# Kernel optimization log

Hardware: AMD Instinct MI355X
Metric: run time of the kernel (lower is better)

Reference implementation:

```python
import jax, jax.numpy as jnp
import numpy as np
import math

B, L, D, H, DFF = 2, 2048, 1024, 16, 4096

def _mha(xq, xkv, Wq, bq, Wk, bk, Wv, bv, Wo, bo, mask, h):
    # xq: [B,Lq,D], xkv: [B,Lk,D], mask: [B,1,Lq,Lk] bool
    b, lq, d = xq.shape
    dk = d // h
    q = (xq @ Wq + bq).reshape(b, lq, h, dk).transpose(0, 2, 1, 3)        # [B,h,Lq,dk]
    k = (xkv @ Wk + bk).reshape(b, -1, h, dk).transpose(0, 2, 1, 3)       # [B,h,Lk,dk]
    v = (xkv @ Wv + bv).reshape(b, -1, h, dk).transpose(0, 2, 1, 3)       # [B,h,Lk,dk]
    scores = jnp.einsum('bhqd,bhkd->bhqk', q, k) / jnp.sqrt(jnp.float32(dk))
    scores = jnp.where(mask, scores, jnp.float32(-1e9))                   # masked_fill(mask==0, -1e9)
    prob = jax.nn.softmax(scores, axis=-1)
    out = jnp.einsum('bhqk,bhkd->bhqd', prob, v)
    out = out.transpose(0, 2, 1, 3).reshape(b, lq, d)
    return out @ Wo + bo

def setup_inputs() -> dict:
    key = jax.random.key(0)
    ks = jax.random.split(key, 16)
    s = 0.02
    inp = {
        'tgt': jax.random.normal(ks[0], (B, L, D), jnp.float32),
        'encoder_out': jax.random.normal(ks[1], (B, L, D), jnp.float32),
        'tgt_mask': jnp.broadcast_to(jnp.tril(jnp.ones((L, L), bool)), (B, 1, L, L)),
        'src_tgt_mask': jnp.ones((B, 1, L, L), bool),
    }
    names = ['sWq','sWk','sWv','sWo','cWq','cWk','cWv','cWo']
    for i, n in enumerate(names):
        inp[n] = s * jax.random.normal(ks[2 + i], (D, D), jnp.float32)
        inp['sb' + n[2] if n[0] == 's' else 'cb' + n[2]] = jnp.zeros((D,), jnp.float32)
    inp['W1'] = s * jax.random.normal(ks[10], (D, DFF), jnp.float32)
    inp['b1'] = jnp.zeros((DFF,), jnp.float32)
    inp['W2'] = s * jax.random.normal(ks[11], (DFF, D), jnp.float32)
    inp['b2'] = jnp.zeros((D,), jnp.float32)
    return inp

def reference(tgt, encoder_out, tgt_mask, src_tgt_mask,
              sWq, sbq, sWk, sbk, sWv, sbv, sWo, sbo,
              cWq, cbq, cWk, cbk, cWv, cbv, cWo, cbo,
              W1, b1, W2, b2):
    # residual 1: masked self-attention (no norm)
    x = tgt + _mha(tgt, tgt, sWq, sbq, sWk, sbk, sWv, sbv, sWo, sbo, tgt_mask, H)
    # residual 2: cross-attention over encoder_out
    x = x + _mha(x, encoder_out, cWq, cbq, cWk, cbk, cWv, cbv, cWo, cbo, src_tgt_mask, H)
    # residual 3: position-wise FFN with ReLU
    x = x + (jax.nn.relu(x @ W1 + b1) @ W2 + b2)
    return x
```

## Files before the change

### kernel.cpp

```cpp
#include <hip/hip_runtime.h>

typedef unsigned short u16;
typedef unsigned int u32;
typedef __attribute__((ext_vector_type(8))) short short8;
typedef __attribute__((ext_vector_type(8))) __bf16 bf16x8;
typedef __attribute__((ext_vector_type(4))) float f32x4;
typedef __attribute__((ext_vector_type(4))) u16 u16x4;
typedef __attribute__((ext_vector_type(2))) u32 u32x2;

#define GLD16(gp, lp) __builtin_amdgcn_global_load_lds( \
    (const __attribute__((address_space(1))) unsigned int*)(gp), \
    (__attribute__((address_space(3))) unsigned int*)(lp), 16, 0, 0)

#if defined(__has_builtin) && __has_builtin(__builtin_amdgcn_exp2f)
#define EXP2(x) __builtin_amdgcn_exp2f(x)
#else
static __device__ __forceinline__ float exp2_asm(float x){
  float r; asm("v_exp_f32 %0, %1" : "=v"(r) : "v"(x)); return r;
}
#define EXP2(x) exp2_asm(x)
#endif

__device__ __forceinline__ float bf2f(u16 u){
  unsigned x = ((unsigned)u) << 16; float f; __builtin_memcpy(&f, &x, 4); return f;
}
__device__ __forceinline__ u16 f2bf(float f){
  unsigned x; __builtin_memcpy(&x, &f, 4);
  x += 0x7fffu + ((x >> 16) & 1u);
  return (u16)(x >> 16);
}
__device__ __forceinline__ u32 pkhi(float lo, float hi){
  u32 a, b; __builtin_memcpy(&a, &lo, 4); __builtin_memcpy(&b, &hi, 4);
  return __builtin_amdgcn_perm(b, a, 0x07060302u);
}
__device__ __forceinline__ f32x4 mfma_bf16(short8 a, short8 b, f32x4 c){
  return __builtin_amdgcn_mfma_f32_16x16x32_bf16(
      __builtin_bit_cast(bf16x8, a), __builtin_bit_cast(bf16x8, b), c, 0, 0, 0);
}

__global__ __launch_bounds__(256) void k_conv(const float* __restrict__ s, u16* __restrict__ d, int n){
  int i4 = (blockIdx.x * 256 + threadIdx.x) * 4;
  if (i4 < n){
    float4 v = *(const float4*)(s + i4);
    u16x4 o; o.x = f2bf(v.x); o.y = f2bf(v.y); o.z = f2bf(v.z); o.w = f2bf(v.w);
    *(u16x4*)(d + i4) = o;
  }
}

__global__ __launch_bounds__(256) void k_transpose(const float* __restrict__ s, u16* __restrict__ d, int K, int N){
  __shared__ float t[32][33];
  int bx = blockIdx.x * 32, by = blockIdx.y * 32;
  int x = threadIdx.x & 31, y = threadIdx.x >> 5;
  #pragma unroll
  for (int i = 0; i < 4; i++)
    t[y + i*8][x] = s[(size_t)(by + y + i*8) * N + bx + x];
  __syncthreads();
  #pragma unroll
  for (int i = 0; i < 4; i++)
    d[(size_t)(bx + y + i*8) * K + by + x] = f2bf(t[x][y + i*8]);
}

struct TP8 { const float* s[8]; u16* d[8]; };
__global__ __launch_bounds__(256) void k_transpose8(TP8 p){
  __shared__ float t[32][33];
  const float* s = p.s[blockIdx.z];
  u16* d = p.d[blockIdx.z];
  int bx = blockIdx.x * 32, by = blockIdx.y * 32;
  int x = threadIdx.x & 31, y = threadIdx.x >> 5;
  #pragma unroll
  for (int i = 0; i < 4; i++)
    t[y + i*8][x] = s[(size_t)(by + y + i*8) * 1024 + bx + x];
  __syncthreads();
  #pragma unroll
  for (int i = 0; i < 4; i++)
    d[(size_t)(bx + y + i*8) * 1024 + by + x] = f2bf(t[x][y + i*8]);
}

__global__ __launch_bounds__(256) void k_packbias(
    const float* __restrict__ sbq, const float* __restrict__ sbk,
    const float* __restrict__ sbv, const float* __restrict__ cbk,
    const float* __restrict__ cbv, float* __restrict__ pbS,
    float* __restrict__ pbC){
  int i = blockIdx.x * 256 + threadIdx.x;
  if (i < 3072) pbS[i] = (i < 1024) ? sbq[i] : (i < 2048 ? sbk[i-1024] : sbv[i-2048]);
  if (i < 2048) pbC[i] = (i < 1024) ? cbk[i] : cbv[i-1024];
}

template<int EPI>
__global__ __launch_bounds__(256, 2) void k_gemm_bt(
    const u16* __restrict__ A, const u16* __restrict__ BT,
    const float* __restrict__ bias, const float* __restrict__ resid,
    float* __restrict__ outF, u16* __restrict__ outB,
    int M, int N, int K, int vt_start, u16* __restrict__ Vt){
  __shared__ u16 As[2][128*32];
  __shared__ u16 Bs[2][128*32];
  int tid = threadIdx.x, wave = tid >> 6, lane = tid & 63;
  int bm = blockIdx.x * 128, bn = blockIdx.y * 128;
  int wm = (wave & 1) * 64, wn = (wave >> 1) * 64;
  int l15 = lane & 15, quad = lane >> 4;

  f32x4 z = {0.f, 0.f, 0.f, 0.f};
  f32x4 acc[4][4];
  #pragma unroll
  for (int a = 0; a < 4; a++)
    #pragma unroll
    for (int b = 0; b < 4; b++) acc[a][b] = z;

  int sr = wave*16 + (lane >> 2);
  int sc = (lane & 3) * 8;
  const u16* Ag = A  + (size_t)(bm + sr) * K + sc;
  const u16* Bg = BT + (size_t)(bn + sr) * K + sc;
  int NK = K >> 5;

  GLD16(Ag,                 &As[0][(wave*16     ) * 32]);
  GLD16(Ag + (size_t)64*K,  &As[0][(wave*16 + 64) * 32]);
  GLD16(Bg,                 &Bs[0][(wave*16     ) * 32]);
  GLD16(Bg + (size_t)64*K,  &Bs[0][(wave*16 + 64) * 32]);

  for (int kt = 0; kt < NK; kt++){
    __syncthreads();
    int cur = kt & 1;
    if (kt + 1 < NK){
      int nb = cur ^ 1, k0 = (kt + 1) * 32;
      GLD16(Ag + k0,                &As[nb][(wave*16     ) * 32]);
      GLD16(Ag + (size_t)64*K + k0, &As[nb][(wave*16 + 64) * 32]);
      GLD16(Bg + k0,                &Bs[nb][(wave*16     ) * 32]);
      GLD16(Bg + (size_t)64*K + k0, &Bs[nb][(wave*16 + 64) * 32]);
    }
    short8 af[4], bf[4];
    #pragma unroll
    for (int mi = 0; mi < 4; mi++)
      af[mi] = *(const short8*)&As[cur][(wm + mi*16 + l15)*32 + quad*8];
    #pragma unroll
    for (int ni = 0; ni < 4; ni++)
      bf[ni] = *(const short8*)&Bs[cur][(wn + ni*16 + l15)*32 + quad*8];
    #pragma unroll
    for (int mi = 0; mi < 4; mi++)
      #pragma unroll
      for (int ni = 0; ni < 4; ni++)
        acc[mi][ni] = mfma_bf16(af[mi], bf[ni], acc[mi][ni]);
  }

  #pragma unroll
  for (int mi = 0; mi < 4; mi++){
    #pragma unroll
    for (int ni = 0; ni < 4; ni++){
      int col = bn + wn + ni*16 + l15;
      float bv = bias[col];
      if (EPI == 0 && col >= vt_start){
        int vc = col - vt_start;
        int hh = vc >> 6, dd = vc & 63;
        int row0 = bm + wm + mi*16 + quad*4;
        int bb = row0 >> 11, ll = row0 & 2047;
        u16x4 vv;
        #pragma unroll
        for (int r = 0; r < 4; r++) vv[r] = f2bf(acc[mi][ni][r] + bv);
        *(u16x4*)&Vt[(((size_t)bb*16 + hh)*64 + dd)*2048 + ll] = vv;
      } else {
        #pragma unroll
        for (int r = 0; r < 4; r++){
          int row = bm + wm + mi*16 + quad*4 + r;
          float v = acc[mi][ni][r] + bv;
          if (EPI == 1) v = v > 0.f ? v : 0.f;
          size_t idx = (size_t)row * N + col;
          if (EPI >= 2) v += resid[idx];
          if (EPI == 2 || EPI == 3) outF[idx] = v;
          if (EPI != 3) outB[idx] = f2bf(v);
        }
      }
    }
  }
}

template<bool CAUSAL>
__global__ __launch_bounds__(256, 2) void k_flash(
    const u16* __restrict__ Q, int ldq,
    const u16* __restrict__ Kg, int ldk,
    const u16* __restrict__ Vt,
    u16* __restrict__ O, int ldo){
  __shared__ u16 Ks[128*64];
  __shared__ u16 Vs[64*128];
  __shared__ u16 Ps[128*128];
  int tid = threadIdx.x, wave = tid >> 6, lane = tid & 63;
  int l15 = lane & 15, quad = lane >> 4;
  int bx = blockIdx.x;
  int qt = CAUSAL ? ((bx & 1) ? (15 - (bx >> 1)) : (bx >> 1)) : bx;
  int bh = blockIdx.y;
  int b = bh >> 4, h = bh & 15;
  size_t bL = (size_t)b * 2048;
  const u16* qp = Q  + (bL + qt*128) * (size_t)ldq + h*64;
  const u16* kp = Kg + bL * (size_t)ldk + h*64;
  const u16* vtp = Vt + (size_t)bh * 64 * 2048;
  int wm = wave * 32;

  const float QSCALE = 0.125f * 1.44269504088896f;
  short8 qf[2][2];
  #pragma unroll
  for (int mi = 0; mi < 2; mi++)
    #pragma unroll
    for (int ks = 0; ks < 2; ks++){
      short8 t = *(const short8*)(qp + (size_t)(wm + mi*16 + l15)*ldq + ks*32 + quad*8);
      #pragma unroll
      for (int j = 0; j < 8; j++)
        t[j] = (short)f2bf(bf2f((u16)t[j]) * QSCALE);
      qf[mi][ks] = t;
    }

  f32x4 z = {0.f, 0.f, 0.f, 0.f};
  f32x4 o[2][4];
  float mrow[2], lrow[2];
  #pragma unroll
  for (int mi = 0; mi < 2; mi++){ mrow[mi] = -3.0e38f; lrow[mi] = 0.f; }
  #pragma unroll
  for (int mi = 0; mi < 2; mi++)
    #pragma unroll
    for (int nd = 0; nd < 4; nd++) o[mi][nd] = z;

  int nkt = CAUSAL ? (qt + 1) : 16;
  for (int kt = 0; kt < nkt; kt++){
    int cg = ((lane & 7) ^ ((lane >> 3) & 7)) * 8;
    #pragma unroll
    for (int i = 0; i < 4; i++){
      int r = i*32 + wave*8 + (lane >> 3);
      GLD16(kp + (size_t)(kt*128 + r) * ldk + cg, &Ks[(i*32 + wave*8) * 64]);
    }
    #pragma unroll
    for (int i = 0; i < 4; i++){
      int d0 = i*16 + wave*4;
      int d = d0 + (lane >> 4);
      int j = lane & 15;
      int chunk = (j & 8) | ((j ^ (d & 7)) & 7);
      GLD16(vtp + (size_t)d*2048 + kt*128 + chunk*8, &Vs[d0*128]);
    }
    __syncthreads();

    f32x4 s[2][8];
    #pragma unroll
    for (int mi = 0; mi < 2; mi++)
      #pragma unroll
      for (int nk = 0; nk < 8; nk++) s[mi][nk] = z;
    #pragma unroll
    for (int ks = 0; ks < 2; ks++){
      short8 kf[8];
      #pragma unroll
      for (int nk = 0; nk < 8; nk++){
        int row = nk*16 + l15;
        kf[nk] = *(const short8*)&Ks[row*64 + (((ks*4 + quad) ^ (row & 7)))*8];
      }
      #pragma unroll
      for (int mi = 0; mi < 2; mi++)
        #pragma unroll
        for (int nk = 0; nk < 8; nk++)
          s[mi][nk] = mfma_bf16(kf[nk], qf[mi][ks], s[mi][nk]);
    }

    if (CAUSAL && kt == qt){
      #pragma unroll
      for (int mi = 0; mi < 2; mi++){
        int q = wm + mi*16 + l15;
        #pragma unroll
        for (int nk = 0; nk < 8; nk++)
          #pragma unroll
          for (int r = 0; r < 4; r++){
            int key = nk*16 + quad*4 + r;
            if (key > q) s[mi][nk][r] = -1e30f;
          }
      }
    }

    #pragma unroll
    for (int mi = 0; mi < 2; mi++){
      float mx = s[mi][0][0];
      #pragma unroll
      for (int nk = 0; nk < 8; nk++)
        #pragma unroll
        for (int r = 0; r < 4; r++) mx = fmaxf(mx, s[mi][nk][r]);
      mx = fmaxf(mx, __shfl_xor(mx, 16));
      mx = fmaxf(mx, __shfl_xor(mx, 32));
      float mnew = fmaxf(mrow[mi], mx);
      float alpha = EXP2(mrow[mi] - mnew);
      mrow[mi] = mnew;
      float ls = 0.f;
      #pragma unroll
      for (int nk = 0; nk < 8; nk++)
        #pragma unroll
        for (int r = 0; r < 4; r++){
          float p = EXP2(s[mi][nk][r] - mnew);
          s[mi][nk][r] = p;
          ls += p;
        }
      ls += __shfl_xor(ls, 16);
      ls += __shfl_xor(ls, 32);
      lrow[mi] = lrow[mi] * alpha + ls;
      #pragma unroll
      for (int r = 0; r < 4; r++){
        float ar = __shfl(alpha, quad*20 + r);
        #pragma unroll
        for (int nd = 0; nd < 4; nd++) o[mi][nd][r] *= ar;
      }
    }

    #pragma unroll
    for (int mi = 0; mi < 2; mi++){
      int row = wm + mi*16 + l15;
      #pragma unroll
      for (int nk = 0; nk < 8; nk++){
        u32x2 pw;
        pw.x = pkhi(s[mi][nk][0], s[mi][nk][1]);
        pw.y = pkhi(s[mi][nk][2], s[mi][nk][3]);
        int c = nk*4 + quad;
        int phys = c ^ (row & 14);
        *(u32x2*)&Ps[row*128 + phys*4] = pw;
      }
    }

    #pragma unroll
    for (int kc = 0; kc < 4; kc++){
      short8 vf[4], pf[2];
      #pragma unroll
      for (int nd = 0; nd < 4; nd++){
        int d = nd*16 + l15;
        int cc = kc*4 + quad;
        int phys = (cc & 8) | ((cc ^ (d & 7)) & 7);
        vf[nd] = *(const short8*)&Vs[d*128 + phys*8];
      }
      #pragma unroll
      for (int mi = 0; mi < 2; mi++){
        int row = wm + mi*16 + l15;
        int c = kc*8 + quad*2;
        int phys = c ^ (row & 14);
        pf[mi] = *(const short8*)&Ps[row*128 + phys*4];
      }
      #pragma unroll
      for (int mi = 0; mi < 2; mi++)
        #pragma unroll
        for (int nd = 0; nd < 4; nd++)
          o[mi][nd] = mfma_bf16(pf[mi], vf[nd], o[mi][nd]);
    }
    __syncthreads();
  }

  u16* op = O + (bL + qt*128) * (size_t)ldo + h*64;
  #pragma unroll
  for (int mi = 0; mi < 2; mi++){
    float invl = 1.f / lrow[mi];
    #pragma unroll
    for (int r = 0; r < 4; r++){
      float ir = __shfl(invl, quad*20 + r);
      #pragma unroll
      for (int nd = 0; nd < 4; nd++)
        op[(size_t)(wm + mi*16 + quad*4 + r)*ldo + nd*16 + l15] = f2bf(o[mi][nd][r] * ir);
    }
  }
}

extern "C" void kernel_launch(void* const* d_in, const int* in_sizes, int n_in,
                              void* d_out, int out_size, void* d_ws, size_t ws_size,
                              hipStream_t stream){
  (void)in_sizes; (void)n_in; (void)out_size; (void)ws_size;
  const float* tgt = (const float*)d_in[0];
  const float* enc = (const float*)d_in[1];
  const float* sWq = (const float*)d_in[4];  const float* sbq = (const float*)d_in[5];
  const float* sWk = (const float*)d_in[6];  const float* sbk = (const float*)d_in[7];
  const float* sWv = (const float*)d_in[8];  const float* sbv = (const float*)d_in[9];
  const float* sWo = (const float*)d_in[10]; const float* sbo = (const float*)d_in[11];
  const float* cWq = (const float*)d_in[12]; const float* cbq = (const float*)d_in[13];
  const float* cWk = (const float*)d_in[14]; const float* cbk = (const float*)d_in[15];
  const float* cWv = (const float*)d_in[16]; const float* cbv = (const float*)d_in[17];
  const float* cWo = (const float*)d_in[18]; const float* cbo = (const float*)d_in[19];
  const float* W1  = (const float*)d_in[20]; const float* b1  = (const float*)d_in[21];
  const float* W2  = (const float*)d_in[22]; const float* b2  = (const float*)d_in[23];
  float* out = (float*)d_out;

  const int M = 4096;
  const int NEVER = 1 << 30;
  char* w = (char*)d_ws;
  auto alloc = [&](size_t bytes)->void*{ void* p = w; w += (bytes + 255) & ~(size_t)255; return p; };
  u16* tb    = (u16*)alloc((size_t)M*1024*2);
  u16* eb    = (u16*)alloc((size_t)M*1024*2);
  u16* qkv   = (u16*)alloc((size_t)M*3072*2);
  u16* ao    = (u16*)alloc((size_t)M*1024*2);
  u16* xb    = (u16*)alloc((size_t)M*1024*2);
  float* x1f = (float*)alloc((size_t)M*1024*4);
  u16* hbuf  = (u16*)alloc((size_t)M*4096*2);
  u16* VtS   = (u16*)alloc((size_t)32*64*2048*2);
  u16* VtC   = (u16*)alloc((size_t)32*64*2048*2);
  u16* sQKVT = (u16*)alloc((size_t)3072*1024*2);
  u16* sWoT  = (u16*)alloc((size_t)1024*1024*2);
  u16* cWqT  = (u16*)alloc((size_t)1024*1024*2);
  u16* cKVT  = (u16*)alloc((size_t)2048*1024*2);
  u16* cWoT  = (u16*)alloc((size_t)1024*1024*2);
  u16* W1T   = (u16*)alloc((size_t)4096*1024*2);
  u16* W2T   = (u16*)alloc((size_t)1024*4096*2);
  float* pbS = (float*)alloc(3072*4);
  float* pbC = (float*)alloc(2048*4);
  u16* cq  = tb;
  u16* ckv = qkv;

  k_conv<<<dim3(4096), 256, 0, stream>>>(tgt, tb, M*1024);
  k_conv<<<dim3(4096), 256, 0, stream>>>(enc, eb, M*1024);
  TP8 tp;
  tp.s[0]=sWq; tp.s[1]=sWk; tp.s[2]=sWv; tp.s[3]=sWo;
  tp.s[4]=cWq; tp.s[5]=cWk; tp.s[6]=cWv; tp.s[7]=cWo;
  tp.d[0]=sQKVT; tp.d[1]=sQKVT+1024*1024; tp.d[2]=sQKVT+2048*1024; tp.d[3]=sWoT;
  tp.d[4]=cWqT; tp.d[5]=cKVT; tp.d[6]=cKVT+1024*1024; tp.d[7]=cWoT;
  k_transpose8<<<dim3(32,32,8), 256, 0, stream>>>(tp);
  k_transpose<<<dim3(128,32), 256, 0, stream>>>(W1, W1T, 1024, 4096);
  k_transpose<<<dim3(32,128), 256, 0, stream>>>(W2, W2T, 4096, 1024);
  k_packbias<<<dim3(12), 256, 0, stream>>>(sbq, sbk, sbv, cbk, cbv, pbS, pbC);

  k_gemm_bt<0><<<dim3(32,24), 256, 0, stream>>>(tb, sQKVT, pbS, nullptr, nullptr, qkv, M, 3072, 1024, 2048, VtS);
  k_flash<true><<<dim3(16,32), 256, 0, stream>>>(qkv, 3072, qkv+1024, 3072, VtS, ao, 1024);
  k_gemm_bt<2><<<dim3(32,8), 256, 0, stream>>>(ao, sWoT, sbo, tgt, x1f, xb, M, 1024, 1024, NEVER, nullptr);

  k_gemm_bt<0><<<dim3(32,8), 256, 0, stream>>>(xb, cWqT, cbq, nullptr, nullptr, cq, M, 1024, 1024, NEVER, nullptr);
  k_gemm_bt<0><<<dim3(32,16), 256, 0, stream>>>(eb, cKVT, pbC, nullptr, nullptr, ckv, M, 2048, 1024, 1024, VtC);
  k_flash<false><<<dim3(16,32), 256, 0, stream>>>(cq, 1024, ckv, 2048, VtC, ao, 1024);
  k_gemm_bt<2><<<dim3(32,8), 256, 0, stream>>>(ao, cWoT, cbo, x1f, x1f, xb, M, 1024, 1024, NEVER, nullptr);

  k_gemm_bt<1><<<dim3(32,32), 256, 0, stream>>>(xb, W1T, b1, nullptr, nullptr, hbuf, M, 4096, 1024, NEVER, nullptr);
  k_gemm_bt<3><<<dim3(32,8), 256, 0, stream>>>(hbuf, W2T, b2, x1f, out, nullptr, M, 1024, 4096, NEVER, nullptr);
}
```

Measured before the change: 575.2 us.

## Triple-buffer GEMM loads and add 64-row tile kernel for N=1024 GEMMs

```diff
diff --git a/kernel.cpp b/kernel.cpp
--- a/kernel.cpp
+++ b/kernel.cpp
@@ -11,6 +11,8 @@
 #define GLD16(gp, lp) __builtin_amdgcn_global_load_lds( \
     (const __attribute__((address_space(1))) unsigned int*)(gp), \
     (__attribute__((address_space(3))) unsigned int*)(lp), 16, 0, 0)
+
+#define WAITCNT_VM(N) asm volatile("s_waitcnt vmcnt(" #N ")" ::: "memory")
 
 #if defined(__has_builtin) && __has_builtin(__builtin_amdgcn_exp2f)
 #define EXP2(x) __builtin_amdgcn_exp2f(x)
@@ -89,11 +91,11 @@
 template<int EPI>
 __global__ __launch_bounds__(256, 2) void k_gemm_bt(
     const u16* __restrict__ A, const u16* __restrict__ BT,
-    const float* __restrict__ bias, const float* __restrict__ resid,
-    float* __restrict__ outF, u16* __restrict__ outB,
+    const float* __restrict__ bias,
+    u16* __restrict__ outB,
     int M, int N, int K, int vt_start, u16* __restrict__ Vt){
-  __shared__ u16 As[2][128*32];
-  __shared__ u16 Bs[2][128*32];
+  __shared__ u16 As[3][128*32];
+  __shared__ u16 Bs[3][128*32];
   int tid = threadIdx.x, wave = tid >> 6, lane = tid & 63;
   int bm = blockIdx.x * 128, bn = blockIdx.y * 128;
   int wm = (wave & 1) * 64, wn = (wave >> 1) * 64;
@@ -112,21 +114,21 @@
   const u16* Bg = BT + (size_t)(bn + sr) * K + sc;
   int NK = K >> 5;
 
-  GLD16(Ag,                 &As[0][(wave*16     ) * 32]);
-  GLD16(Ag + (size_t)64*K,  &As[0][(wave*16 + 64) * 32]);
-  GLD16(Bg,                 &Bs[0][(wave*16     ) * 32]);
-  GLD16(Bg + (size_t)64*K,  &Bs[0][(wave*16 + 64) * 32]);
+  auto stage = [&](int k0, int s){
+    GLD16(Ag + k0,                &As[s][(wave*16     ) * 32]);
+    GLD16(Ag + (size_t)64*K + k0, &As[s][(wave*16 + 64) * 32]);
+    GLD16(Bg + k0,                &Bs[s][(wave*16     ) * 32]);
+    GLD16(Bg + (size_t)64*K + k0, &Bs[s][(wave*16 + 64) * 32]);
+  };
+  stage(0, 0);
+  stage(32, 1);
 
   for (int kt = 0; kt < NK; kt++){
-    __syncthreads();
-    int cur = kt & 1;
-    if (kt + 1 < NK){
-      int nb = cur ^ 1, k0 = (kt + 1) * 32;
-      GLD16(Ag + k0,                &As[nb][(wave*16     ) * 32]);
-      GLD16(Ag + (size_t)64*K + k0, &As[nb][(wave*16 + 64) * 32]);
-      GLD16(Bg + k0,                &Bs[nb][(wave*16     ) * 32]);
-      GLD16(Bg + (size_t)64*K + k0, &Bs[nb][(wave*16 + 64) * 32]);
-    }
+    if (kt + 1 < NK) { WAITCNT_VM(4); } else { WAITCNT_VM(0); }
+    __builtin_amdgcn_s_barrier();
+    int nt = kt + 2;
+    if (nt < NK) stage(nt * 32, nt % 3);
+    int cur = kt % 3;
     short8 af[4], bf[4];
     #pragma unroll
     for (int mi = 0; mi < 4; mi++)
@@ -162,11 +164,81 @@
           int row = bm + wm + mi*16 + quad*4 + r;
           float v = acc[mi][ni][r] + bv;
           if (EPI == 1) v = v > 0.f ? v : 0.f;
-          size_t idx = (size_t)row * N + col;
-          if (EPI >= 2) v += resid[idx];
-          if (EPI == 2 || EPI == 3) outF[idx] = v;
-          if (EPI != 3) outB[idx] = f2bf(v);
+          outB[(size_t)row * N + col] = f2bf(v);
         }
+      }
+    }
+  }
+}
+
+template<int EPI>
+__global__ __launch_bounds__(256, 2) void k_gemm_n64(
+    const u16* __restrict__ A, const u16* __restrict__ BT,
+    const float* __restrict__ bias, const float* __restrict__ resid,
+    float* __restrict__ outF, u16* __restrict__ outB,
+    int M, int N, int K){
+  __shared__ u16 As[3][64*32];
+  __shared__ u16 Bs[3][128*32];
+  int tid = threadIdx.x, wave = tid >> 6, lane = tid & 63;
+  int bm = blockIdx.x * 64, bn = blockIdx.y * 128;
+  int wn = wave * 32;
+  int l15 = lane & 15, quad = lane >> 4;
+
+  f32x4 z = {0.f, 0.f, 0.f, 0.f};
+  f32x4 acc[4][2];
+  #pragma unroll
+  for (int a = 0; a < 4; a++)
+    #pragma unroll
+    for (int b = 0; b < 2; b++) acc[a][b] = z;
+
+  int sr = wave*16 + (lane >> 2);
+  int sc = (lane & 3) * 8;
+  const u16* Ag = A  + (size_t)(bm + sr) * K + sc;
+  const u16* Bg = BT + (size_t)(bn + sr) * K + sc;
+  int NK = K >> 5;
+
+  auto stage = [&](int k0, int s){
+    GLD16(Ag + k0,                &As[s][(wave*16     ) * 32]);
+    GLD16(Bg + k0,                &Bs[s][(wave*16     ) * 32]);
+    GLD16(Bg + (size_t)64*K + k0, &Bs[s][(wave*16 + 64) * 32]);
+  };
+  stage(0, 0);
+  stage(32, 1);
+
+  for (int kt = 0; kt < NK; kt++){
+    if (kt + 1 < NK) { WAITCNT_VM(3); } else { WAITCNT_VM(0); }
+    __builtin_amdgcn_s_barrier();
+    int nt = kt + 2;
+    if (nt < NK) stage(nt * 32, nt % 3);
+    int cur = kt % 3;
+    short8 af[4], bf[2];
+    #pragma unroll
+    for (int mi = 0; mi < 4; mi++)
+      af[mi] = *(const short8*)&As[cur][(mi*16 + l15)*32 + quad*8];
+    #pragma unroll
+    for (int ni = 0; ni < 2; ni++)
+      bf[ni] = *(const short8*)&Bs[cur][(wn + ni*16 + l15)*32 + quad*8];
+    #pragma unroll
+    for (int mi = 0; mi < 4; mi++)
+      #pragma unroll
+      for (int ni = 0; ni < 2; ni++)
+        acc[mi][ni] = mfma_bf16(af[mi], bf[ni], acc[mi][ni]);
+  }
+
+  #pragma unroll
+  for (int mi = 0; mi < 4; mi++){
+    #pragma unroll
+    for (int ni = 0; ni < 2; ni++){
+      int col = bn + wn + ni*16 + l15;
+      float bv = bias[col];
+      #pragma unroll
+      for (int r = 0; r < 4; r++){
+        int row = bm + mi*16 + quad*4 + r;
+        float v = acc[mi][ni][r] + bv;
+        size_t idx = (size_t)row * N + col;
+        if (EPI >= 2) v += resid[idx];
+        if (EPI == 2 || EPI == 3) outF[idx] = v;
+        if (EPI != 3) outB[idx] = f2bf(v);
       }
     }
   }
@@ -409,15 +481,15 @@
   k_transpose<<<dim3(32,128), 256, 0, stream>>>(W2, W2T, 4096, 1024);
   k_packbias<<<dim3(12), 256, 0, stream>>>(sbq, sbk, sbv, cbk, cbv, pbS, pbC);
 
-  k_gemm_bt<0><<<dim3(32,24), 256, 0, stream>>>(tb, sQKVT, pbS, nullptr, nullptr, qkv, M, 3072, 1024, 2048, VtS);
+  k_gemm_bt<0><<<dim3(32,24), 256, 0, stream>>>(tb, sQKVT, pbS, qkv, M, 3072, 1024, 2048, VtS);
   k_flash<true><<<dim3(16,32), 256, 0, stream>>>(qkv, 3072, qkv+1024, 3072, VtS, ao, 1024);
-  k_gemm_bt<2><<<dim3(32,8), 256, 0, stream>>>(ao, sWoT, sbo, tgt, x1f, xb, M, 1024, 1024, NEVER, nullptr);
-
-  k_gemm_bt<0><<<dim3(32,8), 256, 0, stream>>>(xb, cWqT, cbq, nullptr, nullptr, cq, M, 1024, 1024, NEVER, nullptr);
-  k_gemm_bt<0><<<dim3(32,16), 256, 0, stream>>>(eb, cKVT, pbC, nullptr, nullptr, ckv, M, 2048, 1024, 1024, VtC);
+  k_gemm_n64<2><<<dim3(64,8), 256, 0, stream>>>(ao, sWoT, sbo, tgt, x1f, xb, M, 1024, 1024);
+
+  k_gemm_n64<0><<<dim3(64,8), 256, 0, stream>>>(xb, cWqT, cbq, nullptr, nullptr, cq, M, 1024, 1024);
+  k_gemm_bt<0><<<dim3(32,16), 256, 0, stream>>>(eb, cKVT, pbC, ckv, M, 2048, 1024, 1024, VtC);
   k_flash<false><<<dim3(16,32), 256, 0, stream>>>(cq, 1024, ckv, 2048, VtC, ao, 1024);
-  k_gemm_bt<2><<<dim3(32,8), 256, 0, stream>>>(ao, cWoT, cbo, x1f, x1f, xb, M, 1024, 1024, NEVER, nullptr);
-
-  k_gemm_bt<1><<<dim3(32,32), 256, 0, stream>>>(xb, W1T, b1, nullptr, nullptr, hbuf, M, 4096, 1024, NEVER, nullptr);
-  k_gemm_bt<3><<<dim3(32,8), 256, 0, stream>>>(hbuf, W2T, b2, x1f, out, nullptr, M, 1024, 4096, NEVER, nullptr);
-}
+  k_gemm_n64<2><<<dim3(64,8), 256, 0, stream>>>(ao, cWoT, cbo, x1f, x1f, xb, M, 1024, 1024);
+
+  k_gemm_bt<1><<<dim3(32,32), 256, 0, stream>>>(xb, W1T, b1, hbuf, M, 4096, 1024, NEVER, nullptr);
+  k_gemm_n64<3><<<dim3(64,8), 256, 0, stream>>>(hbuf, W2T, b2, x1f, out, nullptr, M, 1024, 4096);
+}
```

New measurement: 579.3 us. About the same (+0.7%).
